# Kernel tuning notes

Hardware: AMD Instinct MI355X
Metric: run time of the kernel (lower is better)

## Reference

```python
import jax, jax.numpy as jnp
import numpy as np

B, S, D, H = 2, 2048, 1024, 16
DK = D // H
MAX_REL = 2047          # clip range for relative distances
REL_DIM = 64            # rel_embedding dim, summed over


def setup_inputs() -> dict:
    key = jax.random.key(0)
    ks = jax.random.split(key, 12)
    sc = 1.0 / np.sqrt(D)
    inp = {
        "q": jax.random.normal(ks[0], (B, S, D), jnp.float32),
        "k": jax.random.normal(ks[1], (B, S, D), jnp.float32),
        "v": jax.random.normal(ks[2], (B, S, D), jnp.float32),
        "Wq": jax.random.normal(ks[3], (D, D), jnp.float32) * sc,
        "bq": jnp.zeros((D,), jnp.float32),
        "Wk": jax.random.normal(ks[4], (D, D), jnp.float32) * sc,
        "bk": jnp.zeros((D,), jnp.float32),
        "Wv": jax.random.normal(ks[5], (D, D), jnp.float32) * sc,
        "bv": jnp.zeros((D,), jnp.float32),
        "Wo": jax.random.normal(ks[6], (D, D), jnp.float32) * sc,
        "bo": jnp.zeros((D,), jnp.float32),
        "rel_table": jax.random.normal(ks[7], (2 * MAX_REL + 1, REL_DIM), jnp.float32) * 0.02,
        "mask": jnp.tril(jnp.ones((1, 1, S, S), jnp.bool_)),  # causal
    }
    return inp


def reference(q, k, v, Wq, bq, Wk, bk, Wv, bv, Wo, bo, rel_table, mask):
    def split_heads(x):
        # [B,S,D] -> [B,H,S,DK]
        return x.reshape(B, -1, H, DK).transpose(0, 2, 1, 3)

    Q = split_heads(q @ Wq + bq)
    K = split_heads(k @ Wk + bk)
    V = split_heads(v @ Wv + bv)

    scores = jnp.einsum("bhqd,bhkd->bhqk", Q, K) / jnp.sqrt(jnp.float32(DK))

    # relative position bias: table[clip(j - i)] summed over rel dim -> [S,S]
    rel_idx = jnp.clip(jnp.arange(S)[None, :] - jnp.arange(S)[:, None],
                       -MAX_REL, MAX_REL) + MAX_REL
    rel_bias = rel_table[rel_idx].sum(-1)  # [S,S]
    scores = scores + rel_bias[None, None]

    scores = jnp.where(mask, scores, jnp.float32(-1e20))
    attn = jax.nn.softmax(scores, axis=-1)

    out = jnp.einsum("bhqk,bhkd->bhqd", attn, V)
    out = out.transpose(0, 2, 1, 3).reshape(B, -1, D)
    return out @ Wo + bo
```

## Files before the change

kernel.cpp:

```cpp
#include <hip/hip_runtime.h>

#define SEQ 2048
#define DIM 1024
#define NH 16
#define HD 64
#define NB 2

typedef __bf16 bf16x8 __attribute__((ext_vector_type(8)));
typedef float f32x4 __attribute__((ext_vector_type(4)));
typedef float f32x4v __attribute__((ext_vector_type(4)));
typedef float f32x4u __attribute__((ext_vector_type(4), aligned(4)));
typedef unsigned short us8 __attribute__((ext_vector_type(8)));
typedef unsigned short us4 __attribute__((ext_vector_type(4)));

#define LOG2E 1.44269504f

__device__ __forceinline__ unsigned short bfbits(float f) {
  __bf16 h = (__bf16)f;
  return __builtin_bit_cast(unsigned short, h);
}

__device__ __forceinline__ void gload16(const unsigned short* g, unsigned short* l) {
  __builtin_amdgcn_global_load_lds(
      (const __attribute__((address_space(1))) unsigned int*)(const void*)g,
      (__attribute__((address_space(3))) unsigned int*)(void*)l, 16, 0, 0);
}

__global__ __launch_bounds__(256) void wconv4_kernel(
    const float* __restrict__ W0, const float* __restrict__ W1,
    const float* __restrict__ W2, const float* __restrict__ W3,
    unsigned short* __restrict__ Wt, const float* __restrict__ rel_table,
    float* __restrict__ relsum, const float* __restrict__ Aq,
    const float* __restrict__ Ak, const float* __restrict__ Av,
    unsigned short* __restrict__ Bq, unsigned short* __restrict__ Bk,
    unsigned short* __restrict__ Bv) {
  int z = blockIdx.z;
  int tid = threadIdx.x;
  if (z == 4) {
    int ti = blockIdx.y * 16 + blockIdx.x;
    int i = ti * 256 + tid;
    if (i < 4095) {
      const f32x4v* row = reinterpret_cast<const f32x4v*>(rel_table + (size_t)i * 64);
      float s = 0.f;
      for (int d = 0; d < 16; ++d) {
        f32x4v v = row[d];
        s += v[0] + v[1] + v[2] + v[3];
      }
      relsum[i] = s * LOG2E - 8.0f;
    }
    return;
  }
  if (z >= 5) {
    const float* src = (z == 5) ? Aq : (z == 6) ? Ak : Av;
    unsigned short* dst = (z == 5) ? Bq : (z == 6) ? Bk : Bv;
    int bid2 = blockIdx.y * 16 + blockIdx.x;
    int c0 = bid2 * 256 + tid;
    for (int j = 0; j < 8; ++j) {
      size_t e = ((size_t)(c0 + j * 65536)) * 8;
      f32x4v v0 = *reinterpret_cast<const f32x4v*>(src + e);
      f32x4v v1 = *reinterpret_cast<const f32x4v*>(src + e + 4);
      us8 o;
      o[0] = bfbits(v0[0]); o[1] = bfbits(v0[1]); o[2] = bfbits(v0[2]); o[3] = bfbits(v0[3]);
      o[4] = bfbits(v1[0]); o[5] = bfbits(v1[1]); o[6] = bfbits(v1[2]); o[7] = bfbits(v1[3]);
      *reinterpret_cast<us8*>(dst + e) = o;
    }
    return;
  }
  __shared__ unsigned short T[64][68];
  const float* W = (z == 0) ? W0 : (z == 1) ? W1 : (z == 2) ? W2 : W3;
  unsigned short* out = Wt + (size_t)z * 1024 * 1024;
  int r0 = blockIdx.y * 64;
  int c0 = blockIdx.x * 64;
  for (int it = 0; it < 4; ++it) {
    int s = tid + it * 256;
    int r = s >> 4;
    int c4 = (s & 15) * 4;
    f32x4v v = *reinterpret_cast<const f32x4v*>(W + (size_t)(r0 + r) * 1024 + c0 + c4);
    us4 o;
    o[0] = bfbits(v[0]); o[1] = bfbits(v[1]); o[2] = bfbits(v[2]); o[3] = bfbits(v[3]);
    *reinterpret_cast<us4*>(&T[r][c4]) = o;
  }
  __syncthreads();
  for (int it = 0; it < 2; ++it) {
    int s = tid + it * 256;
    int n = s >> 3;
    int k8 = (s & 7) * 8;
    us8 o;
    for (int e = 0; e < 8; ++e) o[e] = T[k8 + e][n];
    *reinterpret_cast<us8*>(out + (size_t)(c0 + n) * 1024 + r0 + k8) = o;
  }
}

#define GEMM_CORE(A_, WT_)                                                   \
  __shared__ unsigned short As[2][128 * 64];                                 \
  __shared__ unsigned short Ws[2][64 * 64];                                  \
  int tid = threadIdx.x;                                                     \
  int w = tid >> 6;                                                          \
  int lane = tid & 63;                                                       \
  int lg = lane >> 4;                                                        \
  int li = lane & 15;                                                        \
  int wr = (w >> 1) * 64;                                                    \
  int wc = (w & 1) * 32;                                                     \
  int swz = li & 7;                                                          \
  f32x4 acc[4][2] = {};                                                      \
        \
  int sA0 = tid;                                                             \
  int rA0 = sA0 >> 3, gA0 = (sA0 & 7) ^ (rA0 & 7);                           \
  int sW0 = tid;                                                             \
  int rW0 = sW0 >> 3, gW0 = (sW0 & 7) ^ (rW0 & 7);                           \
  (void)sW0;                                                                 \
  _Pragma("nounroll")                                                        \
  for (int dummy = 0; dummy < 1; ++dummy) {}                                 \
                                    \
  {                                                                          \
    for (int it = 0; it < 4; ++it) {                                         \
      int s = tid + it * 256;                                                \
      int r = s >> 3, g = (s & 7) ^ (r & 7);                                 \
      gload16(A_ + (size_t)(row0 + r) * 1024 + g * 8, &As[0][s * 8]);        \
    }                                                                        \
    for (int it = 0; it < 2; ++it) {                                         \
      int s = tid + it * 256;                                                \
      int r = s >> 3, g = (s & 7) ^ (r & 7);                                 \
      gload16(WT_ + (size_t)(col0 + r) * 1024 + g * 8, &Ws[0][s * 8]);       \
    }                                                                        \
  }                                                                          \
  __syncthreads();                                                           \
  for (int ks = 0; ks < 16; ++ks) {                                          \
    if (ks < 15) {                                                           \
      int k0 = (ks + 1) * 64;                                                \
      int B2 = (ks + 1) & 1;                                                 \
      for (int it = 0; it < 4; ++it) {                                       \
        int s = tid + it * 256;                                              \
        int r = s >> 3, g = (s & 7) ^ (r & 7);                               \
        gload16(A_ + (size_t)(row0 + r) * 1024 + k0 + g * 8, &As[B2][s * 8]);\
      }                                                                      \
      for (int it = 0; it < 2; ++it) {                                       \
        int s = tid + it * 256;                                              \
        int r = s >> 3, g = (s & 7) ^ (r & 7);                               \
        gload16(WT_ + (size_t)(col0 + r) * 1024 + k0 + g * 8, &Ws[B2][s * 8]);\
      }                                                                      \
    }                                                                        \
    int B = ks & 1;                                                          \
    for (int kk = 0; kk < 2; ++kk) {                                         \
      bf16x8 af[4], bfr[2];                                                  \
      int gidx = ((kk << 2) | lg) ^ swz;                                     \
      for (int m = 0; m < 4; ++m)                                            \
        af[m] = *reinterpret_cast<const bf16x8*>(                            \
            &As[B][(wr + m * 16 + li) * 64 + gidx * 8]);                     \
      for (int n = 0; n < 2; ++n)                                            \
        bfr[n] = *reinterpret_cast<const bf16x8*>(                           \
            &Ws[B][(wc + n * 16 + li) * 64 + gidx * 8]);                     \
      for (int m = 0; m < 4; ++m)                                            \
        for (int n = 0; n < 2; ++n)                                          \
          acc[m][n] = __builtin_amdgcn_mfma_f32_16x16x32_bf16(               \
              af[m], bfr[n], acc[m][n], 0, 0, 0);                            \
    }                                                                        \
    __syncthreads();                                                         \
  }                                                                          \
  (void)rA0; (void)gA0; (void)rW0; (void)gW0; (void)sA0;

__global__ __launch_bounds__(256) void gemm_qkv_kernel(
    const unsigned short* __restrict__ Aq, const unsigned short* __restrict__ Ak,
    const unsigned short* __restrict__ Av, const unsigned short* __restrict__ WTb,
    const float* __restrict__ bq, const float* __restrict__ bk,
    const float* __restrict__ bv, unsigned short* __restrict__ Qb,
    unsigned short* __restrict__ Kb, unsigned short* __restrict__ Vt,
    float qscale) {
  int o = (blockIdx.x & 7) * 192 + (blockIdx.x >> 3);
  int z = o >> 9;
  int r2 = o & 511;
  int row0 = (r2 >> 4) * 128;
  int col0 = (r2 & 15) * 64;
  const unsigned short* A = (z == 0) ? Aq : (z == 1) ? Ak : Av;
  const unsigned short* WT = WTb + (size_t)z * 1024 * 1024;
  const float* bias = (z == 0) ? bq : (z == 1) ? bk : bv;
  float oscale = (z == 0) ? qscale : 1.0f;

  GEMM_CORE(A, WT)

  for (int m = 0; m < 4; ++m)
    for (int n = 0; n < 2; ++n) {
      int row = row0 + wr + m * 16 + lg * 4;
      int col = col0 + wc + n * 16 + li;
      float v4[4];
      for (int r = 0; r < 4; ++r) v4[r] = (acc[m][n][r] + bias[col]) * oscale;
      if (z == 2) {
        int bb = row >> 11, seq = row & 2047;
        int hh = col >> 6, dk = col & 63;
        us4 o4;
        o4[0] = bfbits(v4[0]); o4[1] = bfbits(v4[1]);
        o4[2] = bfbits(v4[2]); o4[3] = bfbits(v4[3]);
        *reinterpret_cast<us4*>(
            Vt + ((size_t)(bb * NH + hh) * HD + dk) * SEQ + seq) = o4;
      } else {
        unsigned short* Cp = (z == 0) ? Qb : Kb;
        for (int r = 0; r < 4; ++r)
          Cp[(size_t)(row + r) * 1024 + col] = bfbits(v4[r]);
      }
    }
}

__global__ __launch_bounds__(256) void gemm_out_kernel(
    const unsigned short* __restrict__ A, const unsigned short* __restrict__ WT,
    const float* __restrict__ bias, float* __restrict__ Cp) {
  int o = ((blockIdx.x & 7) << 6) | (blockIdx.x >> 3);
  int col0 = (o & 15) * 64;
  int row0 = (o >> 4) * 128;

  GEMM_CORE(A, WT)

  for (int m = 0; m < 4; ++m)
    for (int n = 0; n < 2; ++n)
      for (int r = 0; r < 4; ++r) {
        int row = row0 + wr + m * 16 + lg * 4 + r;
        int col = col0 + wc + n * 16 + li;
        Cp[(size_t)row * 1024 + col] = acc[m][n][r] + bias[col];
      }
}

__global__ __launch_bounds__(256) void attn_kernel(
    const unsigned short* __restrict__ Qb, const unsigned short* __restrict__ Kb,
    const unsigned short* __restrict__ Vt, const float* __restrict__ relsum,
    unsigned short* __restrict__ Ob) {
  int r0_ = blockIdx.x >> 3;
  int xcd = blockIdx.x & 7;
  int qt = 31 - (r0_ >> 2);
  int bh = xcd * 4 + (r0_ & 3);
  int h = bh & 15;
  int b = bh >> 4;

  int tid = threadIdx.x;
  int w = tid >> 6;
  int lane = tid & 63;
  int lg = lane >> 4;
  int li = lane & 15;

  __shared__ unsigned short Ks[64][72];
  __shared__ unsigned short VtF[64 * 72];
  __shared__ __bf16 Ps[4][16][72];

  int key0 = tid >> 3;
  int cg0 = (tid & 7) * 8;
  int dk0 = tid >> 3;
  int k8 = (tid & 7) * 8;
  const unsigned short* kptr = Kb + ((size_t)(b * SEQ + key0)) * DIM + h * HD + cg0;
  const unsigned short* vtp = Vt + ((size_t)(b * NH + h) * HD + dk0) * SEQ + k8;

  unsigned vidx0 = ((unsigned)(dk0 * 72 + k8)) ^ ((((unsigned)dk0 >> 3) & 7u) << 3);
  unsigned vidx1 = ((unsigned)((dk0 + 32) * 72 + k8)) ^
                   ((((unsigned)(dk0 + 32) >> 3) & 7u) << 3);

  us8 krg0, krg1, vrg0, vrg1;

#define LOAD_REGS(TT)                                                     \
  {                                                                       \
    size_t koff = (size_t)(TT) * 64 * DIM;                                \
    krg0 = *reinterpret_cast<const us8*>(kptr + koff);                    \
    krg1 = *reinterpret_cast<const us8*>(kptr + koff + 32 * DIM);         \
    vrg0 = *reinterpret_cast<const us8*>(vtp + (TT) * 64);                \
    vrg1 = *reinterpret_cast<const us8*>(vtp + 32 * SEQ + (TT) * 64);     \
  }

#define WRITE_TILE()                                                      \
  {                                                                       \
    *reinterpret_cast<us8*>(&Ks[key0][cg0]) = krg0;                       \
    *reinterpret_cast<us8*>(&Ks[key0 + 32][cg0]) = krg1;                  \
    *reinterpret_cast<us8*>(&VtF[vidx0]) = vrg0;                          \
    *reinterpret_cast<us8*>(&VtF[vidx1]) = vrg1;                          \
  }

  LOAD_REGS(0);

  int qrow = qt * 64 + w * 16 + li;
  const unsigned short* qb = Qb + ((size_t)(b * SEQ + qrow)) * DIM + h * HD;
  bf16x8 qa0 = *reinterpret_cast<const bf16x8*>(qb + lg * 8);
  bf16x8 qa1 = *reinterpret_cast<const bf16x8*>(qb + 32 + lg * 8);

  f32x4 o_acc[4] = {};
  float l_row[4] = {0.f, 0.f, 0.f, 0.f};
  int i0 = qt * 64 + w * 16 + lg * 4;

  for (int t = 0; t <= qt; ++t) {
    __syncthreads();
    WRITE_TILE();
    __syncthreads();

    if (t < qt) LOAD_REGS(t + 1);

    f32x4 s_acc[4] = {};
    __builtin_amdgcn_s_setprio(1);
    for (int kk = 0; kk < 2; ++kk) {
      bf16x8 qa = kk ? qa1 : qa0;
      for (int n = 0; n < 4; ++n) {
        bf16x8 kb = *reinterpret_cast<const bf16x8*>(&Ks[n * 16 + li][kk * 32 + lg * 8]);
        s_acc[n] = __builtin_amdgcn_mfma_f32_16x16x32_bf16(qa, kb, s_acc[n], 0, 0, 0);
      }
    }
    __builtin_amdgcn_s_setprio(0);

    int Cbase = (t - qt) * 64 - (w * 16 + lg * 4) + li + 2047;
    if (t == qt) {
      for (int n = 0; n < 4; ++n) {
        int Cn = Cbase + n * 16;
        f32x4u rel4 = *reinterpret_cast<const f32x4u*>(&relsum[Cn - 3]);
        for (int r = 0; r < 4; ++r) {
          float sv = s_acc[n][r] + rel4[3 - r];
          sv = (Cn - r > 2047) ? -1e30f : sv;
          float e = exp2f(sv);
          s_acc[n][r] = e;
          l_row[r] += e;
        }
      }
    } else {
      for (int n = 0; n < 4; ++n) {
        int Cn = Cbase + n * 16;
        f32x4u rel4 = *reinterpret_cast<const f32x4u*>(&relsum[Cn - 3]);
        for (int r = 0; r < 4; ++r) {
          float e = exp2f(s_acc[n][r] + rel4[3 - r]);
          s_acc[n][r] = e;
          l_row[r] += e;
        }
      }
    }

    for (int n = 0; n < 4; ++n)
      for (int r = 0; r < 4; ++r)
        Ps[w][lg * 4 + r][n * 16 + li] = (__bf16)s_acc[n][r];
    asm volatile("s_waitcnt lgkmcnt(0)" ::: "memory");
    __builtin_amdgcn_sched_barrier(0);

    __builtin_amdgcn_s_setprio(1);
    for (int kk = 0; kk < 2; ++kk) {
      bf16x8 pa = *reinterpret_cast<const bf16x8*>(&Ps[w][li][kk * 32 + lg * 8]);
      for (int n = 0; n < 4; ++n) {
        int dk = n * 16 + li;
        unsigned idx = ((unsigned)(dk * 72 + kk * 32 + lg * 8)) ^
                       ((((unsigned)dk >> 3) & 7u) << 3);
        bf16x8 vb = *reinterpret_cast<const bf16x8*>(&VtF[idx]);
        o_acc[n] = __builtin_amdgcn_mfma_f32_16x16x32_bf16(pa, vb, o_acc[n], 0, 0, 0);
      }
    }
    __builtin_amdgcn_s_setprio(0);
  }

  for (int msk = 1; msk < 16; msk <<= 1)
    for (int r = 0; r < 4; ++r) l_row[r] += __shfl_xor(l_row[r], msk);
  float inv_l[4];
  for (int r = 0; r < 4; ++r) inv_l[r] = 1.f / l_row[r];
  for (int n = 0; n < 4; ++n)
    for (int r = 0; r < 4; ++r) {
      int row = i0 + r;
      int dk = n * 16 + li;
      Ob[((size_t)(b * SEQ + row)) * DIM + h * HD + dk] =
          bfbits(o_acc[n][r] * inv_l[r]);
    }
#undef LOAD_REGS
#undef WRITE_TILE
}

extern "C" void kernel_launch(void* const* d_in, const int* in_sizes, int n_in,
                              void* d_out, int out_size, void* d_ws, size_t ws_size,
                              hipStream_t stream) {
  const float* q = (const float*)d_in[0];
  const float* k = (const float*)d_in[1];
  const float* v = (const float*)d_in[2];
  const float* Wq = (const float*)d_in[3];
  const float* bq = (const float*)d_in[4];
  const float* Wk = (const float*)d_in[5];
  const float* bk = (const float*)d_in[6];
  const float* Wv = (const float*)d_in[7];
  const float* bv = (const float*)d_in[8];
  const float* Wo = (const float*)d_in[9];
  const float* bo = (const float*)d_in[10];
  const float* rel = (const float*)d_in[11];

  char* ws = (char*)d_ws;
  const size_t MATB = (size_t)NB * SEQ * DIM * sizeof(unsigned short);
  const size_t WTE = (size_t)DIM * DIM;
  unsigned short* Qb = (unsigned short*)(ws);
  unsigned short* Kb = (unsigned short*)(ws + MATB);
  unsigned short* Vt = (unsigned short*)(ws + 2 * MATB);
  unsigned short* Ob = (unsigned short*)(ws + 3 * MATB);
  float* relsum = (float*)(ws + 4 * MATB);
  unsigned short* WT = (unsigned short*)(ws + 4 * MATB + 65536);

  unsigned short* Abq = (unsigned short*)d_out;
  unsigned short* Abk = (unsigned short*)d_out + (size_t)NB * SEQ * DIM;
  unsigned short* Abv = Ob;

  wconv4_kernel<<<dim3(16, 16, 8), 256, 0, stream>>>(
      Wq, Wk, Wv, Wo, WT, rel, relsum, q, k, v, Abq, Abk, Abv);

  const float qscale = 0.125f * LOG2E;
  gemm_qkv_kernel<<<dim3(1536), 256, 0, stream>>>(Abq, Abk, Abv, WT, bq, bk, bv,
                                                  Qb, Kb, Vt, qscale);

  attn_kernel<<<dim3(1024), 256, 0, stream>>>(Qb, Kb, Vt, relsum, Ob);

  gemm_out_kernel<<<dim3(512), 256, 0, stream>>>(Ob, WT + 3 * WTE, bo, (float*)d_out);
}
```

Baseline: 120.9 us.

## Double-buffer attention K/V tiles with direct global-to-LDS async loads

The attention kernel now loads K and V^T tiles straight into LDS with global_load_lds into two ping-pong buffers, instead of staging them through registers and writing LDS. This drops the register round-trip and one barrier per iteration, and lets the next tile's loads overlap the current tile's compute. It uses an XOR-swizzled 64-wide layout with no padding, matching the GEMM. LDS use grows to two buffers per operand. It also removes dead setup code from the GEMM macro.

New measurement: 121.0 us, median of 3. Within noise of the previous version (+0.1%).

```diff
diff --git a/kernel.cpp b/kernel.cpp
--- a/kernel.cpp
+++ b/kernel.cpp
@@ -103,15 +103,6 @@
   int wc = (w & 1) * 32;                                                     \
   int swz = li & 7;                                                          \
   f32x4 acc[4][2] = {};                                                      \
-        \
-  int sA0 = tid;                                                             \
-  int rA0 = sA0 >> 3, gA0 = (sA0 & 7) ^ (rA0 & 7);                           \
-  int sW0 = tid;                                                             \
-  int rW0 = sW0 >> 3, gW0 = (sW0 & 7) ^ (rW0 & 7);                           \
-  (void)sW0;                                                                 \
-  _Pragma("nounroll")                                                        \
-  for (int dummy = 0; dummy < 1; ++dummy) {}                                 \
-                                    \
   {                                                                          \
     for (int it = 0; it < 4; ++it) {                                         \
       int s = tid + it * 256;                                                \
@@ -156,8 +147,7 @@
               af[m], bfr[n], acc[m][n], 0, 0, 0);                            \
     }                                                                        \
     __syncthreads();                                                         \
-  }                                                                          \
-  (void)rA0; (void)gA0; (void)rW0; (void)gW0; (void)sA0;
+  }
 
 __global__ __launch_bounds__(256) void gemm_qkv_kernel(
     const unsigned short* __restrict__ Aq, const unsigned short* __restrict__ Ak,
@@ -235,41 +225,26 @@
   int lg = lane >> 4;
   int li = lane & 15;
 
-  __shared__ unsigned short Ks[64][72];
-  __shared__ unsigned short VtF[64 * 72];
+  __shared__ unsigned short KsF[2][64 * 64];
+  __shared__ unsigned short VtF[2][64 * 64];
   __shared__ __bf16 Ps[4][16][72];
 
-  int key0 = tid >> 3;
-  int cg0 = (tid & 7) * 8;
-  int dk0 = tid >> 3;
-  int k8 = (tid & 7) * 8;
-  const unsigned short* kptr = Kb + ((size_t)(b * SEQ + key0)) * DIM + h * HD + cg0;
-  const unsigned short* vtp = Vt + ((size_t)(b * NH + h) * HD + dk0) * SEQ + k8;
-
-  unsigned vidx0 = ((unsigned)(dk0 * 72 + k8)) ^ ((((unsigned)dk0 >> 3) & 7u) << 3);
-  unsigned vidx1 = ((unsigned)((dk0 + 32) * 72 + k8)) ^
-                   ((((unsigned)(dk0 + 32) >> 3) & 7u) << 3);
-
-  us8 krg0, krg1, vrg0, vrg1;
-
-#define LOAD_REGS(TT)                                                     \
-  {                                                                       \
-    size_t koff = (size_t)(TT) * 64 * DIM;                                \
-    krg0 = *reinterpret_cast<const us8*>(kptr + koff);                    \
-    krg1 = *reinterpret_cast<const us8*>(kptr + koff + 32 * DIM);         \
-    vrg0 = *reinterpret_cast<const us8*>(vtp + (TT) * 64);                \
-    vrg1 = *reinterpret_cast<const us8*>(vtp + 32 * SEQ + (TT) * 64);     \
-  }
-
-#define WRITE_TILE()                                                      \
-  {                                                                       \
-    *reinterpret_cast<us8*>(&Ks[key0][cg0]) = krg0;                       \
-    *reinterpret_cast<us8*>(&Ks[key0 + 32][cg0]) = krg1;                  \
-    *reinterpret_cast<us8*>(&VtF[vidx0]) = vrg0;                          \
-    *reinterpret_cast<us8*>(&VtF[vidx1]) = vrg1;                          \
-  }
-
-  LOAD_REGS(0);
+  const unsigned short* kbase = Kb + ((size_t)(b)*SEQ) * DIM + h * HD;
+  const unsigned short* vbase = Vt + (size_t)(b * NH + h) * HD * SEQ;
+
+#define STAGE(TT, B)                                                        \
+  {                                                                         \
+    for (int it = 0; it < 2; ++it) {                                        \
+      int s = tid + it * 256;                                               \
+      int r = s >> 3, g = (s & 7) ^ (r & 7);                                \
+      gload16(kbase + (size_t)((TT)*64 + r) * DIM + g * 8, &KsF[B][s * 8]); \
+    }                                                                       \
+    for (int it = 0; it < 2; ++it) {                                        \
+      int s = tid + it * 256;                                               \
+      int dk = s >> 3, g = (s & 7) ^ (dk & 7);                              \
+      gload16(vbase + (size_t)dk * SEQ + (TT)*64 + g * 8, &VtF[B][s * 8]);  \
+    }                                                                       \
+  }
 
   int qrow = qt * 64 + w * 16 + li;
   const unsigned short* qb = Qb + ((size_t)(b * SEQ + qrow)) * DIM + h * HD;
@@ -279,20 +254,23 @@
   f32x4 o_acc[4] = {};
   float l_row[4] = {0.f, 0.f, 0.f, 0.f};
   int i0 = qt * 64 + w * 16 + lg * 4;
+  int swz = li & 7;
+
+  STAGE(0, 0);
+  __syncthreads();
 
   for (int t = 0; t <= qt; ++t) {
-    __syncthreads();
-    WRITE_TILE();
-    __syncthreads();
-
-    if (t < qt) LOAD_REGS(t + 1);
+    int B = t & 1;
+    if (t < qt) STAGE(t + 1, B ^ 1);
 
     f32x4 s_acc[4] = {};
     __builtin_amdgcn_s_setprio(1);
     for (int kk = 0; kk < 2; ++kk) {
       bf16x8 qa = kk ? qa1 : qa0;
+      int gidx = ((kk << 2) | lg) ^ swz;
       for (int n = 0; n < 4; ++n) {
-        bf16x8 kb = *reinterpret_cast<const bf16x8*>(&Ks[n * 16 + li][kk * 32 + lg * 8]);
+        bf16x8 kb = *reinterpret_cast<const bf16x8*>(
+            &KsF[B][(n * 16 + li) * 64 + gidx * 8]);
         s_acc[n] = __builtin_amdgcn_mfma_f32_16x16x32_bf16(qa, kb, s_acc[n], 0, 0, 0);
       }
     }
@@ -332,15 +310,16 @@
     __builtin_amdgcn_s_setprio(1);
     for (int kk = 0; kk < 2; ++kk) {
       bf16x8 pa = *reinterpret_cast<const bf16x8*>(&Ps[w][li][kk * 32 + lg * 8]);
+      int gidx = ((kk << 2) | lg) ^ swz;
       for (int n = 0; n < 4; ++n) {
-        int dk = n * 16 + li;
-        unsigned idx = ((unsigned)(dk * 72 + kk * 32 + lg * 8)) ^
-                       ((((unsigned)dk >> 3) & 7u) << 3);
-        bf16x8 vb = *reinterpret_cast<const bf16x8*>(&VtF[idx]);
+        bf16x8 vb = *reinterpret_cast<const bf16x8*>(
+            &VtF[B][(n * 16 + li) * 64 + gidx * 8]);
         o_acc[n] = __builtin_amdgcn_mfma_f32_16x16x32_bf16(pa, vb, o_acc[n], 0, 0, 0);
       }
     }
     __builtin_amdgcn_s_setprio(0);
+
+    __syncthreads();
   }
 
   for (int msk = 1; msk < 16; msk <<= 1)
@@ -354,8 +333,7 @@
       Ob[((size_t)(b * SEQ + row)) * DIM + h * HD + dk] =
           bfbits(o_acc[n][r] * inv_l[r]);
     }
-#undef LOAD_REGS
-#undef WRITE_TILE
+#undef STAGE
 }
 
 extern "C" void kernel_launch(void* const* d_in, const int* in_sizes, int n_in,
```

## Split long causal query tiles across two blocks and merge partials

Applied to the files above, without the earlier changes.

Query tiles in the upper half of the causal sequence are split into two KV chunks, each handled by its own block. Each chunk writes unnormalized fp32 partial outputs and row sums into scratch space, and a new reduce kernel adds the pairs, normalizes and writes bf16. The aim is to shorten the longest per-block work and improve load balance and tail behaviour across the grid. In exchange it adds a kernel launch and extra fp32 scratch traffic. Merging partials by plain addition is only correct if both chunks use the same fixed softmax reference value. Dead code in the GEMM macro is also removed.

Result: slower. 133.1 us (+10.1%).

```diff
diff --git a/kernel.cpp b/kernel.cpp
--- a/kernel.cpp
+++ b/kernel.cpp
@@ -103,15 +103,6 @@
   int wc = (w & 1) * 32;                                                     \
   int swz = li & 7;                                                          \
   f32x4 acc[4][2] = {};                                                      \
-        \
-  int sA0 = tid;                                                             \
-  int rA0 = sA0 >> 3, gA0 = (sA0 & 7) ^ (rA0 & 7);                           \
-  int sW0 = tid;                                                             \
-  int rW0 = sW0 >> 3, gW0 = (sW0 & 7) ^ (rW0 & 7);                           \
-  (void)sW0;                                                                 \
-  _Pragma("nounroll")                                                        \
-  for (int dummy = 0; dummy < 1; ++dummy) {}                                 \
-                                    \
   {                                                                          \
     for (int it = 0; it < 4; ++it) {                                         \
       int s = tid + it * 256;                                                \
@@ -156,8 +147,7 @@
               af[m], bfr[n], acc[m][n], 0, 0, 0);                            \
     }                                                                        \
     __syncthreads();                                                         \
-  }                                                                          \
-  (void)rA0; (void)gA0; (void)rW0; (void)gW0; (void)sA0;
+  }
 
 __global__ __launch_bounds__(256) void gemm_qkv_kernel(
     const unsigned short* __restrict__ Aq, const unsigned short* __restrict__ Ak,
@@ -221,13 +211,25 @@
 __global__ __launch_bounds__(256) void attn_kernel(
     const unsigned short* __restrict__ Qb, const unsigned short* __restrict__ Kb,
     const unsigned short* __restrict__ Vt, const float* __restrict__ relsum,
-    unsigned short* __restrict__ Ob) {
-  int r0_ = blockIdx.x >> 3;
+    unsigned short* __restrict__ Ob, float* __restrict__ PartO,
+    float* __restrict__ PartL) {
+  int rr = blockIdx.x >> 3;
   int xcd = blockIdx.x & 7;
-  int qt = 31 - (r0_ >> 2);
-  int bh = xcd * 4 + (r0_ & 3);
+  int bh = xcd * 4 + (rr & 3);
+  int c = rr >> 2;
   int h = bh & 15;
   int b = bh >> 4;
+  int qt, t0, t1, slot;
+  if (c < 32) {
+    qt = 31 - (c >> 1);
+    int chunk = c & 1;
+    if (chunk == 0) { t0 = 0; t1 = 15; } else { t0 = 16; t1 = qt; }
+    slot = (bh * 16 + (qt - 16)) * 2 + chunk;
+  } else {
+    qt = 47 - c;
+    t0 = 0; t1 = qt;
+    slot = -1;
+  }
 
   int tid = threadIdx.x;
   int w = tid >> 6;
@@ -269,7 +271,7 @@
     *reinterpret_cast<us8*>(&VtF[vidx1]) = vrg1;                          \
   }
 
-  LOAD_REGS(0);
+  LOAD_REGS(t0);
 
   int qrow = qt * 64 + w * 16 + li;
   const unsigned short* qb = Qb + ((size_t)(b * SEQ + qrow)) * DIM + h * HD;
@@ -280,12 +282,12 @@
   float l_row[4] = {0.f, 0.f, 0.f, 0.f};
   int i0 = qt * 64 + w * 16 + lg * 4;
 
-  for (int t = 0; t <= qt; ++t) {
+  for (int t = t0; t <= t1; ++t) {
     __syncthreads();
     WRITE_TILE();
     __syncthreads();
 
-    if (t < qt) LOAD_REGS(t + 1);
+    if (t < t1) LOAD_REGS(t + 1);
 
     f32x4 s_acc[4] = {};
     __builtin_amdgcn_s_setprio(1);
@@ -345,17 +347,59 @@
 
   for (int msk = 1; msk < 16; msk <<= 1)
     for (int r = 0; r < 4; ++r) l_row[r] += __shfl_xor(l_row[r], msk);
-  float inv_l[4];
-  for (int r = 0; r < 4; ++r) inv_l[r] = 1.f / l_row[r];
-  for (int n = 0; n < 4; ++n)
-    for (int r = 0; r < 4; ++r) {
-      int row = i0 + r;
-      int dk = n * 16 + li;
-      Ob[((size_t)(b * SEQ + row)) * DIM + h * HD + dk] =
-          bfbits(o_acc[n][r] * inv_l[r]);
-    }
+
+  int i0l = w * 16 + lg * 4;
+  if (slot < 0) {
+    float inv_l[4];
+    for (int r = 0; r < 4; ++r) inv_l[r] = 1.f / l_row[r];
+    for (int n = 0; n < 4; ++n)
+      for (int r = 0; r < 4; ++r) {
+        int row = i0 + r;
+        int dk = n * 16 + li;
+        Ob[((size_t)(b * SEQ + row)) * DIM + h * HD + dk] =
+            bfbits(o_acc[n][r] * inv_l[r]);
+      }
+  } else {
+    float* po = PartO + (size_t)slot * 4096;
+    for (int n = 0; n < 4; ++n)
+      for (int r = 0; r < 4; ++r)
+        po[(i0l + r) * 64 + n * 16 + li] = o_acc[n][r];
+    if (li == 0)
+      for (int r = 0; r < 4; ++r)
+        PartL[(size_t)slot * 64 + i0l + r] = l_row[r];
+  }
 #undef LOAD_REGS
 #undef WRITE_TILE
+}
+
+__global__ __launch_bounds__(256) void attn_reduce_kernel(
+    const float* __restrict__ PartO, const float* __restrict__ PartL,
+    unsigned short* __restrict__ Ob) {
+  int bid = blockIdx.x;
+  int bh = bid >> 4;
+  int qtidx = bid & 15;
+  int b = bh >> 4;
+  int h = bh & 15;
+  int tid = threadIdx.x;
+  int row = tid >> 2;
+  int cs = (tid & 3) * 16;
+  size_t s0 = ((size_t)(bh * 16 + qtidx)) * 2;
+  const float* p0 = PartO + s0 * 4096;
+  const float* p1 = p0 + 4096;
+  float l = PartL[s0 * 64 + row] + PartL[(s0 + 1) * 64 + row];
+  float inv = 1.f / l;
+  int grow = (16 + qtidx) * 64 + row;
+  unsigned short* ob = Ob + ((size_t)(b * SEQ + grow)) * DIM + h * HD + cs;
+  for (int j = 0; j < 4; ++j) {
+    f32x4v a = *reinterpret_cast<const f32x4v*>(p0 + row * 64 + cs + j * 4);
+    f32x4v d = *reinterpret_cast<const f32x4v*>(p1 + row * 64 + cs + j * 4);
+    us4 o;
+    o[0] = bfbits((a[0] + d[0]) * inv);
+    o[1] = bfbits((a[1] + d[1]) * inv);
+    o[2] = bfbits((a[2] + d[2]) * inv);
+    o[3] = bfbits((a[3] + d[3]) * inv);
+    *reinterpret_cast<us4*>(ob + j * 4) = o;
+  }
 }
 
 extern "C" void kernel_launch(void* const* d_in, const int* in_sizes, int n_in,
@@ -383,10 +427,12 @@
   unsigned short* Ob = (unsigned short*)(ws + 3 * MATB);
   float* relsum = (float*)(ws + 4 * MATB);
   unsigned short* WT = (unsigned short*)(ws + 4 * MATB + 65536);
+  float* PartL = (float*)(ws + 4 * MATB + 65536 + 4 * WTE * 2);
 
   unsigned short* Abq = (unsigned short*)d_out;
   unsigned short* Abk = (unsigned short*)d_out + (size_t)NB * SEQ * DIM;
   unsigned short* Abv = Ob;
+  float* PartO = (float*)d_out;
 
   wconv4_kernel<<<dim3(16, 16, 8), 256, 0, stream>>>(
       Wq, Wk, Wv, Wo, WT, rel, relsum, q, k, v, Abq, Abk, Abv);
@@ -395,7 +441,8 @@
   gemm_qkv_kernel<<<dim3(1536), 256, 0, stream>>>(Abq, Abk, Abv, WT, bq, bk, bv,
                                                   Qb, Kb, Vt, qscale);
 
-  attn_kernel<<<dim3(1024), 256, 0, stream>>>(Qb, Kb, Vt, relsum, Ob);
+  attn_kernel<<<dim3(1536), 256, 0, stream>>>(Qb, Kb, Vt, relsum, Ob, PartO, PartL);
+  attn_reduce_kernel<<<dim3(512), 256, 0, stream>>>(PartO, PartL, Ob);
 
   gemm_out_kernel<<<dim3(512), 256, 0, stream>>>(Ob, WT + 3 * WTE, bo, (float*)d_out);
 }
```
